# Kernel optimization log

Measured on AMD Instinct MI355X. Metric: run time of the kernel, lower is better.

## Reference

```python
import jax, jax.numpy as jnp
import numpy as np

DIM = 1024
NUM_HEADS = 8
HEAD_DIM = 64
INNER = NUM_HEADS * HEAD_DIM  # 512


def setup_inputs() -> dict:
    key = jax.random.key(0)
    ks = jax.random.split(key, 7)
    B, N, M = 8, 512, 4096
    x = jax.random.normal(ks[0], (B, N, DIM), dtype=jnp.float32)
    context = jax.random.normal(ks[1], (B, M, DIM), dtype=jnp.float32)
    s_in = 1.0 / np.sqrt(DIM)
    s_inner = 1.0 / np.sqrt(INNER)
    # Linear weights stored as [in, out] for x @ W
    Wq = jax.random.normal(ks[2], (DIM, INNER), dtype=jnp.float32) * s_in
    Wk = jax.random.normal(ks[3], (DIM, INNER), dtype=jnp.float32) * s_in
    Wv = jax.random.normal(ks[4], (DIM, INNER), dtype=jnp.float32) * s_in
    Wo = jax.random.normal(ks[5], (INNER, DIM), dtype=jnp.float32) * s_inner
    bo = jax.random.normal(ks[6], (DIM,), dtype=jnp.float32) * 0.01
    return {"x": x, "context": context, "Wq": Wq, "Wk": Wk, "Wv": Wv, "Wo": Wo, "bo": bo}


def reference(x, context, Wq, Wk, Wv, Wo, bo):
    B, N, _ = x.shape
    M = context.shape[1]
    scale = HEAD_DIM ** -0.5
    # project and split heads: [B, H, N, D]
    q = (x @ Wq).reshape(B, N, NUM_HEADS, HEAD_DIM).transpose(0, 2, 1, 3)
    k = (context @ Wk).reshape(B, M, NUM_HEADS, HEAD_DIM).transpose(0, 2, 1, 3)
    v = (context @ Wv).reshape(B, M, NUM_HEADS, HEAD_DIM).transpose(0, 2, 1, 3)
    # full attention matrix [B, H, N, M] as in the original module
    attn = jax.nn.softmax(jnp.einsum('bhnd,bhmd->bhnm', q, k) * scale, axis=-1)
    out = jnp.einsum('bhnm,bhmd->bhnd', attn, v)  # [B, H, N, D]
    out = out.transpose(0, 2, 1, 3).reshape(B, N, INNER)
    return out @ Wo + bo
```

## Files before the change

### kernel.cpp

```cpp
#include <hip/hip_runtime.h>
#include <hip/hip_bf16.h>

#define B_SZ 8
#define N_Q 512
#define M_KV 4096
#define DIM 1024
#define INNER 512
#define NHEADS 8
#define HDIM 64

typedef __attribute__((ext_vector_type(4))) float floatx4;
typedef __attribute__((ext_vector_type(8))) short shortx8;
typedef __attribute__((ext_vector_type(4))) short shortx4;

__device__ inline unsigned short f2bf(float f) {
  union { float f; unsigned u; } x; x.f = f;
  unsigned r = x.u + 0x7FFFu + ((x.u >> 16) & 1u);
  return (unsigned short)(r >> 16);
}

__device__ inline shortx8 cvt8(floatx4 a, floatx4 b) {
  shortx8 h;
  h[0] = (short)f2bf(a[0]); h[1] = (short)f2bf(a[1]);
  h[2] = (short)f2bf(a[2]); h[3] = (short)f2bf(a[3]);
  h[4] = (short)f2bf(b[0]); h[5] = (short)f2bf(b[1]);
  h[6] = (short)f2bf(b[2]); h[7] = (short)f2bf(b[3]);
  return h;
}

__device__ inline void gload16(const void* g, void* l) {
  __builtin_amdgcn_global_load_lds(
      (const __attribute__((address_space(1))) void*)g,
      (__attribute__((address_space(3))) void*)l, 16, 0, 0);
}

__global__ void k_transpose_bf16(const float* __restrict__ W,
                                 unsigned short* __restrict__ Wt,
                                 int K, int N) {
  __shared__ unsigned short t[32][36];
  const int kt = blockIdx.x * 32, nt = blockIdx.y * 32;
  const int tr = threadIdx.x >> 3;
  const int tc = (threadIdx.x & 7) * 4;
  floatx4 v = *reinterpret_cast<const floatx4*>(&W[(long)(kt + tr) * N + nt + tc]);
  #pragma unroll
  for (int j = 0; j < 4; ++j) t[tr][tc + j] = f2bf(v[j]);
  __syncthreads();
  shortx4 o;
  #pragma unroll
  for (int j = 0; j < 4; ++j) o[j] = (short)t[tc + j][tr];
  *reinterpret_cast<shortx4*>(&Wt[(long)(nt + tr) * K + kt + tc]) = o;
}

__global__ __launch_bounds__(256, 3)
void k_gemm_kv(const float* __restrict__ Actx,
               const unsigned short* __restrict__ Wkvt,
               unsigned short* __restrict__ Kh,
               unsigned short* __restrict__ Vt) {
  __shared__ unsigned short As[2][128 * 32];
  __shared__ unsigned short Bs[2][128 * 32];
  const int tid = threadIdx.x;
  const int lane = tid & 63;
  const int w = tid >> 6;
  const int wr = w >> 1, wc = w & 1;
  const int fr = lane & 15, fc = lane >> 4;

  const int L = ((blockIdx.x & 7) << 8) + (blockIdx.x >> 3);
  const int mt = L >> 3, nt = L & 7;
  const long arow0 = (long)mt << 7;
  const long bcol0 = (long)nt << 7;

  const int arow = tid >> 1;
  const int ahalf = tid & 1;
  const int aswz = (arow >> 1) & 3;
  const int as0 = ((2 * ahalf) ^ aswz) * 8;
  const int as1 = ((2 * ahalf + 1) ^ aswz) * 8;
  const int brl = lane >> 2;
  const int bpos = lane & 3;

  floatx4 acc[4][4] = {};

  {
    const float* s = Actx + (arow0 + arow) * 1024 + ahalf * 16;
    floatx4 a0 = *reinterpret_cast<const floatx4*>(s);
    floatx4 a1 = *reinterpret_cast<const floatx4*>(s + 4);
    floatx4 a2 = *reinterpret_cast<const floatx4*>(s + 8);
    floatx4 a3 = *reinterpret_cast<const floatx4*>(s + 12);
    #pragma unroll
    for (int j = 0; j < 2; ++j) {
      int row = (w * 2 + j) * 16 + brl;
      int c = bpos ^ ((row >> 1) & 3);
      gload16(Wkvt + (bcol0 + row) * 1024 + c * 8, &Bs[0][(w * 2 + j) * 512]);
    }
    *reinterpret_cast<shortx8*>(&As[0][arow * 32 + as0]) = cvt8(a0, a1);
    *reinterpret_cast<shortx8*>(&As[0][arow * 32 + as1]) = cvt8(a2, a3);
  }
  __syncthreads();

  for (int i = 0; i < 32; ++i) {
    const int cur = i & 1;
    const bool more = i < 31;
    floatx4 a0, a1, a2, a3;
    if (more) {
      const float* s = Actx + (arow0 + arow) * 1024 + (i + 1) * 32 + ahalf * 16;
      a0 = *reinterpret_cast<const floatx4*>(s);
      a1 = *reinterpret_cast<const floatx4*>(s + 4);
      a2 = *reinterpret_cast<const floatx4*>(s + 8);
      a3 = *reinterpret_cast<const floatx4*>(s + 12);
      #pragma unroll
      for (int j = 0; j < 2; ++j) {
        int row = (w * 2 + j) * 16 + brl;
        int c = bpos ^ ((row >> 1) & 3);
        gload16(Wkvt + (bcol0 + row) * 1024 + (i + 1) * 32 + c * 8,
                &Bs[cur ^ 1][(w * 2 + j) * 512]);
      }
    }

    shortx8 af[4], bf[4];
    #pragma unroll
    for (int rb = 0; rb < 4; ++rb) {
      int row = wr * 64 + rb * 16 + fr;
      af[rb] = *reinterpret_cast<const shortx8*>(
          &As[cur][row * 32 + ((fc ^ ((row >> 1) & 3)) * 8)]);
    }
    #pragma unroll
    for (int cb = 0; cb < 4; ++cb) {
      int row = wc * 64 + cb * 16 + fr;
      bf[cb] = *reinterpret_cast<const shortx8*>(
          &Bs[cur][row * 32 + ((fc ^ ((row >> 1) & 3)) * 8)]);
    }
    __builtin_amdgcn_s_setprio(1);
    #pragma unroll
    for (int rb = 0; rb < 4; ++rb) {
      #pragma unroll
      for (int cb = 0; cb < 4; ++cb)
        acc[rb][cb] = __builtin_amdgcn_mfma_f32_16x16x32_bf16(
            af[rb], bf[cb], acc[rb][cb], 0, 0, 0);
    }
    __builtin_amdgcn_s_setprio(0);

    if (more) {
      *reinterpret_cast<shortx8*>(&As[cur ^ 1][arow * 32 + as0]) = cvt8(a0, a1);
      *reinterpret_cast<shortx8*>(&As[cur ^ 1][arow * 32 + as1]) = cvt8(a2, a3);
    }
    __syncthreads();
  }

  #pragma unroll
  for (int rb = 0; rb < 4; ++rb) {
    #pragma unroll
    for (int cb = 0; cb < 4; ++cb) {
      long gr0 = arow0 + wr * 64 + rb * 16 + fc * 4;
      long gc = bcol0 + wc * 64 + cb * 16 + fr;
      long b = gr0 >> 12, m = gr0 & 4095;
      if (gc < 512) {
        long h = gc >> 6, d = gc & 63;
        #pragma unroll
        for (int r = 0; r < 4; ++r)
          Kh[((((b * 8 + h) << 12) + m + r) << 6) + d] = f2bf(acc[rb][cb][r]);
      } else {
        long h = (gc - 512) >> 6, d = (gc - 512) & 63;
        shortx4 hv;
        #pragma unroll
        for (int r = 0; r < 4; ++r) hv[r] = (short)f2bf(acc[rb][cb][r]);
        *reinterpret_cast<shortx4*>(&Vt[(((b * 8 + h) * 64 + d) << 12) + m]) = hv;
      }
    }
  }
}

template<int MODE, bool ABF, int NCOL, int MBITS>
__global__ __launch_bounds__(512, 4)
void k_gemm(const void* __restrict__ Ap, const unsigned short* __restrict__ Bt,
            void* __restrict__ Cout, const float* __restrict__ bias,
            int M, int N, int K, float oscale) {
  __shared__ unsigned short As[2][128 * 32];
  __shared__ unsigned short Bs[2][256 * 32];
  const int tid = threadIdx.x;
  const int lane = tid & 63;
  const int w = tid >> 6;
  const int wr = w >> 2, wc = w & 3;

  const int cpx = gridDim.x >> 3;
  const int L = (blockIdx.x & 7) * cpx + (blockIdx.x >> 3);
  const long arow0 = (long)(L / NCOL) * 128;
  const long bcol0 = (long)(L % NCOL) * 256;

  const float* Af = (const float*)Ap;
  const unsigned short* Ah = (const unsigned short*)Ap;

  const int lsub = lane >> 2;
  const int lchunk = (lane & 3) ^ ((lane >> 3) & 3);
  const long brow0 = bcol0 + (w * 2 + 0) * 16 + lsub;
  const long brow1 = bcol0 + (w * 2 + 1) * 16 + lsub;
  const long ahrow = arow0 + w * 16 + lsub;
  const int arow = tid >> 2;
  const int acseg = tid & 3;
  const int aswz = arow * 32 + ((acseg ^ ((arow >> 1) & 3)) * 8);

  floatx4 acc[4][4] = {};

  #define STAGE_B(buf, kt)                                                   \
    {                                                                        \
      gload16(Bt + brow0 * K + (kt) + lchunk * 8, &Bs[buf][(w * 2) * 512]);  \
      gload16(Bt + brow1 * K + (kt) + lchunk * 8,                            \
              &Bs[buf][(w * 2 + 1) * 512]);                                  \
    }
  #define STAGE_AH(buf, kt) \
    gload16(Ah + ahrow * K + (kt) + lchunk * 8, &As[buf][w * 512]);

  if (ABF) {
    STAGE_AH(0, 0);
  } else {
    const float* src = Af + (arow0 + arow) * (long)K + acseg * 8;
    floatx4 a0 = *reinterpret_cast<const floatx4*>(src);
    floatx4 a1 = *reinterpret_cast<const floatx4*>(src + 4);
    *reinterpret_cast<shortx8*>(&As[0][aswz]) = cvt8(a0, a1);
  }
  STAGE_B(0, 0);
  __syncthreads();

  const int NK = K >> 5;
  for (int i = 0; i < NK; ++i) {
    const int cur = i & 1;
    const bool more = (i + 1) < NK;
    floatx4 a0, a1;
    if (more) {
      const long ktn = (long)(i + 1) << 5;
      if (ABF) {
        STAGE_AH(cur ^ 1, ktn);
      } else {
        const float* src = Af + (arow0 + arow) * (long)K + ktn + acseg * 8;
        a0 = *reinterpret_cast<const floatx4*>(src);
        a1 = *reinterpret_cast<const floatx4*>(src + 4);
      }
      STAGE_B(cur ^ 1, ktn);
    }

    shortx8 af[4], bf[4];
    #pragma unroll
    for (int rb = 0; rb < 4; ++rb) {
      int row = wr * 64 + rb * 16 + (lane & 15);
      af[rb] = *reinterpret_cast<const shortx8*>(
          &As[cur][row * 32 + (((lane >> 4) ^ ((row >> 1) & 3)) * 8)]);
    }
    #pragma unroll
    for (int cb = 0; cb < 4; ++cb) {
      int row = wc * 64 + cb * 16 + (lane & 15);
      bf[cb] = *reinterpret_cast<const shortx8*>(
          &Bs[cur][row * 32 + (((lane >> 4) ^ ((row >> 1) & 3)) * 8)]);
    }
    #pragma unroll
    for (int rb = 0; rb < 4; ++rb) {
      #pragma unroll
      for (int cb = 0; cb < 4; ++cb)
        acc[rb][cb] = __builtin_amdgcn_mfma_f32_16x16x32_bf16(
            af[rb], bf[cb], acc[rb][cb], 0, 0, 0);
    }

    if (more && !ABF)
      *reinterpret_cast<shortx8*>(&As[cur ^ 1][aswz]) = cvt8(a0, a1);
    __syncthreads();
  }
  #undef STAGE_B
  #undef STAGE_AH

  #pragma unroll
  for (int rb = 0; rb < 4; ++rb) {
    #pragma unroll
    for (int cb = 0; cb < 4; ++cb) {
      long gr0 = arow0 + wr * 64 + rb * 16 + (lane >> 4) * 4;
      long gc  = bcol0 + wc * 64 + cb * 16 + (lane & 15);
      if (MODE == 0) {
        float bv = bias[gc];
        #pragma unroll
        for (int r = 0; r < 4; ++r)
          ((float*)Cout)[(gr0 + r) * N + gc] = acc[rb][cb][r] + bv;
      } else if (MODE == 2) {
        long b = gr0 >> MBITS, m = gr0 & ((1 << MBITS) - 1);
        long h = gc >> 6, d = gc & 63;
        #pragma unroll
        for (int r = 0; r < 4; ++r)
          ((unsigned short*)Cout)[((((b * 8 + h) << MBITS) + m + r) << 6) + d] =
              f2bf(acc[rb][cb][r] * oscale);
      }
    }
  }
}

__global__ __launch_bounds__(256, 2)
void k_attn(const unsigned short* __restrict__ Qh,
            const unsigned short* __restrict__ Kh,
            const unsigned short* __restrict__ Vt,
            unsigned short* __restrict__ Aout) {
  __shared__ unsigned short Ks[64][72];
  __shared__ unsigned short Vs[64][72];
  __shared__ unsigned short QPs[64][72];
  const int tid = threadIdx.x;
  const int lane = tid & 63;
  const int w = tid >> 6;
  const int wg = blockIdx.x;
  const int bh = wg & 63;
  const int qt = wg >> 6;
  const int b = bh >> 3, h = bh & 7;

  const unsigned short* Qbase = Qh + (((long)bh << 9) + qt * 64) * 64;
  const unsigned short* Kbase = Kh + (((long)bh) << 18);
  const unsigned short* Vbase = Vt + (((long)bh) << 18);

  const int sr = tid >> 2;
  const int sc = (tid & 3) * 16;

  {
    const unsigned short* src = Qbase + sr * 64 + sc;
    *reinterpret_cast<shortx8*>(&QPs[sr][sc]) =
        *reinterpret_cast<const shortx8*>(src);
    *reinterpret_cast<shortx8*>(&QPs[sr][sc + 8]) =
        *reinterpret_cast<const shortx8*>(src + 8);
  }
  {
    const unsigned short* ksrc = Kbase + sr * 64 + sc;
    *reinterpret_cast<shortx8*>(&Ks[sr][sc]) =
        *reinterpret_cast<const shortx8*>(ksrc);
    *reinterpret_cast<shortx8*>(&Ks[sr][sc + 8]) =
        *reinterpret_cast<const shortx8*>(ksrc + 8);
    const unsigned short* vsrc = Vbase + ((long)sr << 12) + sc;
    *reinterpret_cast<shortx8*>(&Vs[sr][sc]) =
        *reinterpret_cast<const shortx8*>(vsrc);
    *reinterpret_cast<shortx8*>(&Vs[sr][sc + 8]) =
        *reinterpret_cast<const shortx8*>(vsrc + 8);
  }
  __syncthreads();

  shortx8 qf[2];
  qf[0] = *reinterpret_cast<const shortx8*>(
      &QPs[w * 16 + (lane & 15)][(lane >> 4) * 8]);
  qf[1] = *reinterpret_cast<const shortx8*>(
      &QPs[w * 16 + (lane & 15)][32 + (lane >> 4) * 8]);

  floatx4 o_acc[4] = {};
  float l_part[4] = {0.f, 0.f, 0.f, 0.f};
  shortx8 kpre[2], vpre[2];

  for (int mt = 0; mt < M_KV / 64; ++mt) {
    if (mt < M_KV / 64 - 1) {
      const unsigned short* ksrc = Kbase + ((mt + 1) * 64 + sr) * 64 + sc;
      kpre[0] = *reinterpret_cast<const shortx8*>(ksrc);
      kpre[1] = *reinterpret_cast<const shortx8*>(ksrc + 8);
      const unsigned short* vsrc = Vbase + ((long)sr << 12) + (mt + 1) * 64 + sc;
      vpre[0] = *reinterpret_cast<const shortx8*>(vsrc);
      vpre[1] = *reinterpret_cast<const shortx8*>(vsrc + 8);
    }

    floatx4 s[4];
    #pragma unroll
    for (int cb = 0; cb < 4; ++cb) {
      shortx8 k0 = *reinterpret_cast<const shortx8*>(
          &Ks[cb * 16 + (lane & 15)][(lane >> 4) * 8]);
      shortx8 k1 = *reinterpret_cast<const shortx8*>(
          &Ks[cb * 16 + (lane & 15)][32 + (lane >> 4) * 8]);
      floatx4 z = {};
      z = __builtin_amdgcn_mfma_f32_16x16x32_bf16(qf[0], k0, z, 0, 0, 0);
      s[cb] = __builtin_amdgcn_mfma_f32_16x16x32_bf16(qf[1], k1, z, 0, 0, 0);
    }

    #pragma unroll
    for (int cb = 0; cb < 4; ++cb) {
      #pragma unroll
      for (int r = 0; r < 4; ++r) {
        float pv = __expf(s[cb][r]);
        l_part[r] += pv;
        QPs[w * 16 + (lane >> 4) * 4 + r][cb * 16 + (lane & 15)] = f2bf(pv);
      }
    }

    #pragma unroll
    for (int kk = 0; kk < 2; ++kk) {
      shortx8 pf = *reinterpret_cast<const shortx8*>(
          &QPs[w * 16 + (lane & 15)][kk * 32 + (lane >> 4) * 8]);
      #pragma unroll
      for (int db = 0; db < 4; ++db) {
        shortx8 vf = *reinterpret_cast<const shortx8*>(
            &Vs[db * 16 + (lane & 15)][kk * 32 + (lane >> 4) * 8]);
        o_acc[db] = __builtin_amdgcn_mfma_f32_16x16x32_bf16(
            pf, vf, o_acc[db], 0, 0, 0);
      }
    }

    __syncthreads();
    if (mt < M_KV / 64 - 1) {
      *reinterpret_cast<shortx8*>(&Ks[sr][sc]) = kpre[0];
      *reinterpret_cast<shortx8*>(&Ks[sr][sc + 8]) = kpre[1];
      *reinterpret_cast<shortx8*>(&Vs[sr][sc]) = vpre[0];
      *reinterpret_cast<shortx8*>(&Vs[sr][sc + 8]) = vpre[1];
      __syncthreads();
    }
  }

  float inv[4];
  #pragma unroll
  for (int r = 0; r < 4; ++r) {
    float l = l_part[r];
    l += __shfl_xor(l, 1);
    l += __shfl_xor(l, 2);
    l += __shfl_xor(l, 4);
    l += __shfl_xor(l, 8);
    inv[r] = 1.f / l;
  }
  #pragma unroll
  for (int db = 0; db < 4; ++db) {
    #pragma unroll
    for (int r = 0; r < 4; ++r) {
      int n = qt * 64 + w * 16 + (lane >> 4) * 4 + r;
      long idx = ((long)(b * N_Q + n)) * INNER + h * HDIM + db * 16 + (lane & 15);
      Aout[idx] = f2bf(o_acc[db][r] * inv[r]);
    }
  }
}

extern "C" void kernel_launch(void* const* d_in, const int* in_sizes, int n_in,
                              void* d_out, int out_size, void* d_ws, size_t ws_size,
                              hipStream_t stream) {
  const float* x   = (const float*)d_in[0];
  const float* ctx = (const float*)d_in[1];
  const float* Wq  = (const float*)d_in[2];
  const float* Wk  = (const float*)d_in[3];
  const float* Wv  = (const float*)d_in[4];
  const float* Wo  = (const float*)d_in[5];
  const float* bo  = (const float*)d_in[6];
  float* out = (float*)d_out;

  char* ws = (char*)d_ws;
  unsigned short* Qh   = (unsigned short*)(ws);
  unsigned short* Kh   = (unsigned short*)(ws + (4ull  << 20));
  unsigned short* Vt   = (unsigned short*)(ws + (36ull << 20));
  unsigned short* Aat  = (unsigned short*)(ws + (68ull << 20));
  unsigned short* Wqt  = (unsigned short*)(ws + (72ull << 20));
  unsigned short* Wkvt = (unsigned short*)(ws + (73ull << 20));
  unsigned short* Wot  = (unsigned short*)(ws + (75ull << 20));

  k_transpose_bf16<<<dim3(DIM / 32, INNER / 32), dim3(256), 0, stream>>>(
      Wq, Wqt, DIM, INNER);
  k_transpose_bf16<<<dim3(DIM / 32, INNER / 32), dim3(256), 0, stream>>>(
      Wk, Wkvt, DIM, INNER);
  k_transpose_bf16<<<dim3(DIM / 32, INNER / 32), dim3(256), 0, stream>>>(
      Wv, Wkvt + (size_t)INNER * DIM, DIM, INNER);
  k_transpose_bf16<<<dim3(INNER / 32, DIM / 32), dim3(256), 0, stream>>>(
      Wo, Wot, INNER, DIM);

  k_gemm<2, false, 2, 9><<<dim3(64), dim3(512), 0, stream>>>(
      x, Wqt, Qh, nullptr, B_SZ * N_Q, INNER, DIM, 0.125f);

  k_gemm_kv<<<dim3(2048), dim3(256), 0, stream>>>(ctx, Wkvt, Kh, Vt);

  k_attn<<<dim3(B_SZ * NHEADS * (N_Q / 64)), dim3(256), 0, stream>>>(Qh, Kh, Vt, Aat);

  k_gemm<0, true, 4, 0><<<dim3(128), dim3(512), 0, stream>>>(
      Aat, Wot, out, bo, B_SZ * N_Q, DIM, INNER, 1.0f);
}
```

Baseline: 246.9 us.

## Pre-convert context to bf16 and stage both KV GEMM operands via direct LDS loads

A new elementwise kernel converts the whole fp32 context tensor to bf16 in workspace before the K/V projection GEMM. The GEMM then loads both A and B tiles with global_load_lds, with no register staging or in-loop conversion, and its launch bound is raised to 4 blocks per SM. This removes conversion work and register pressure from the GEMM main loop. The cost is an extra full pass over the large context tensor: it is read once in fp32 and written once in bf16, and the converted copy is then read back. Workspace offsets for the weights are moved to make room, and the bf16 context shares space with the later attention output buffer.

```diff
diff --git a/kernel.cpp b/kernel.cpp
--- a/kernel.cpp
+++ b/kernel.cpp
@@ -32,6 +32,16 @@
   __builtin_amdgcn_global_load_lds(
       (const __attribute__((address_space(1))) void*)g,
       (__attribute__((address_space(3))) void*)l, 16, 0, 0);
+}
+
+__global__ void k_cvt_bf16(const float* __restrict__ src,
+                           unsigned short* __restrict__ dst, long n) {
+  long stride = (long)gridDim.x * 256 * 8;
+  for (long i = ((long)blockIdx.x * 256 + threadIdx.x) * 8; i < n; i += stride) {
+    floatx4 a = *reinterpret_cast<const floatx4*>(src + i);
+    floatx4 b = *reinterpret_cast<const floatx4*>(src + i + 4);
+    *reinterpret_cast<shortx8*>(dst + i) = cvt8(a, b);
+  }
 }
 
 __global__ void k_transpose_bf16(const float* __restrict__ W,
@@ -51,8 +61,8 @@
   *reinterpret_cast<shortx4*>(&Wt[(long)(nt + tr) * K + kt + tc]) = o;
 }
 
-__global__ __launch_bounds__(256, 3)
-void k_gemm_kv(const float* __restrict__ Actx,
+__global__ __launch_bounds__(256, 4)
+void k_gemm_kv(const unsigned short* __restrict__ Ah,
                const unsigned short* __restrict__ Wkvt,
                unsigned short* __restrict__ Kh,
                unsigned short* __restrict__ Vt) {
@@ -69,51 +79,30 @@
   const long arow0 = (long)mt << 7;
   const long bcol0 = (long)nt << 7;
 
-  const int arow = tid >> 1;
-  const int ahalf = tid & 1;
-  const int aswz = (arow >> 1) & 3;
-  const int as0 = ((2 * ahalf) ^ aswz) * 8;
-  const int as1 = ((2 * ahalf + 1) ^ aswz) * 8;
-  const int brl = lane >> 2;
-  const int bpos = lane & 3;
+  const int grow = lane >> 2;
+  const int gpos = lane & 3;
 
   floatx4 acc[4][4] = {};
 
-  {
-    const float* s = Actx + (arow0 + arow) * 1024 + ahalf * 16;
-    floatx4 a0 = *reinterpret_cast<const floatx4*>(s);
-    floatx4 a1 = *reinterpret_cast<const floatx4*>(s + 4);
-    floatx4 a2 = *reinterpret_cast<const floatx4*>(s + 8);
-    floatx4 a3 = *reinterpret_cast<const floatx4*>(s + 12);
-    #pragma unroll
-    for (int j = 0; j < 2; ++j) {
-      int row = (w * 2 + j) * 16 + brl;
-      int c = bpos ^ ((row >> 1) & 3);
-      gload16(Wkvt + (bcol0 + row) * 1024 + c * 8, &Bs[0][(w * 2 + j) * 512]);
-    }
-    *reinterpret_cast<shortx8*>(&As[0][arow * 32 + as0]) = cvt8(a0, a1);
-    *reinterpret_cast<shortx8*>(&As[0][arow * 32 + as1]) = cvt8(a2, a3);
-  }
+  #define STAGE(buf, kt)                                                      \
+    {                                                                         \
+      _Pragma("unroll")                                                       \
+      for (int g = 0; g < 2; ++g) {                                           \
+        const int rl = w * 32 + g * 16 + grow;                                \
+        const int cc = gpos ^ ((rl >> 1) & 3);                                \
+        gload16(Ah + (arow0 + rl) * 1024 + (kt) + cc * 8,                     \
+                &As[buf][(w * 32 + g * 16) * 32]);                            \
+        gload16(Wkvt + (bcol0 + rl) * 1024 + (kt) + cc * 8,                   \
+                &Bs[buf][(w * 32 + g * 16) * 32]);                            \
+      }                                                                       \
+    }
+
+  STAGE(0, 0);
   __syncthreads();
 
   for (int i = 0; i < 32; ++i) {
     const int cur = i & 1;
-    const bool more = i < 31;
-    floatx4 a0, a1, a2, a3;
-    if (more) {
-      const float* s = Actx + (arow0 + arow) * 1024 + (i + 1) * 32 + ahalf * 16;
-      a0 = *reinterpret_cast<const floatx4*>(s);
-      a1 = *reinterpret_cast<const floatx4*>(s + 4);
-      a2 = *reinterpret_cast<const floatx4*>(s + 8);
-      a3 = *reinterpret_cast<const floatx4*>(s + 12);
-      #pragma unroll
-      for (int j = 0; j < 2; ++j) {
-        int row = (w * 2 + j) * 16 + brl;
-        int c = bpos ^ ((row >> 1) & 3);
-        gload16(Wkvt + (bcol0 + row) * 1024 + (i + 1) * 32 + c * 8,
-                &Bs[cur ^ 1][(w * 2 + j) * 512]);
-      }
-    }
+    if (i < 31) STAGE(cur ^ 1, (i + 1) << 5);
 
     shortx8 af[4], bf[4];
     #pragma unroll
@@ -137,13 +126,9 @@
             af[rb], bf[cb], acc[rb][cb], 0, 0, 0);
     }
     __builtin_amdgcn_s_setprio(0);
-
-    if (more) {
-      *reinterpret_cast<shortx8*>(&As[cur ^ 1][arow * 32 + as0]) = cvt8(a0, a1);
-      *reinterpret_cast<shortx8*>(&As[cur ^ 1][arow * 32 + as1]) = cvt8(a2, a3);
-    }
     __syncthreads();
   }
+  #undef STAGE
 
   #pragma unroll
   for (int rb = 0; rb < 4; ++rb) {
@@ -433,10 +418,14 @@
   unsigned short* Qh   = (unsigned short*)(ws);
   unsigned short* Kh   = (unsigned short*)(ws + (4ull  << 20));
   unsigned short* Vt   = (unsigned short*)(ws + (36ull << 20));
+  unsigned short* ctxh = (unsigned short*)(ws + (68ull << 20));
   unsigned short* Aat  = (unsigned short*)(ws + (68ull << 20));
-  unsigned short* Wqt  = (unsigned short*)(ws + (72ull << 20));
-  unsigned short* Wkvt = (unsigned short*)(ws + (73ull << 20));
-  unsigned short* Wot  = (unsigned short*)(ws + (75ull << 20));
+  unsigned short* Wqt  = (unsigned short*)(ws + (132ull << 20));
+  unsigned short* Wkvt = (unsigned short*)(ws + (133ull << 20));
+  unsigned short* Wot  = (unsigned short*)(ws + (135ull << 20));
+
+  k_cvt_bf16<<<dim3(2048), dim3(256), 0, stream>>>(
+      ctx, ctxh, (long)B_SZ * M_KV * DIM);
 
   k_transpose_bf16<<<dim3(DIM / 32, INNER / 32), dim3(256), 0, stream>>>(
       Wq, Wqt, DIM, INNER);
@@ -450,7 +439,7 @@
   k_gemm<2, false, 2, 9><<<dim3(64), dim3(512), 0, stream>>>(
       x, Wqt, Qh, nullptr, B_SZ * N_Q, INNER, DIM, 0.125f);
 
-  k_gemm_kv<<<dim3(2048), dim3(256), 0, stream>>>(ctx, Wkvt, Kh, Vt);
+  k_gemm_kv<<<dim3(2048), dim3(256), 0, stream>>>(ctxh, Wkvt, Kh, Vt);
 
   k_attn<<<dim3(B_SZ * NHEADS * (N_Q / 64)), dim3(256), 0, stream>>>(Qh, Kh, Vt, Aat);
 
```

Result: slower. 256.0 us (+3.7%).
